# Performance work log

Measured on AMD Instinct MI355X. Metric: run time of the kernel, lower is better.

Reference implementation:

```python
import jax, jax.numpy as jnp
import numpy as np

N_NODES = 50000
N_EDGES = 800000
N_REL = 16
D = 64          # entity_dim == relation_dim == n_hidden
NEG_SLOPE = 0.01  # torch F.leaky_relu default


def setup_inputs() -> dict:
    key = jax.random.key(0)
    ks = jax.random.split(key, 12)
    s = 1.0 / np.sqrt(D)
    return {
        "node_ids": jnp.arange(N_NODES, dtype=jnp.int64) if jax.config.jax_enable_x64 else jnp.arange(N_NODES, dtype=jnp.int32),
        "relation_ids": jax.random.randint(ks[0], (N_EDGES,), 0, N_REL),
        "src": jax.random.randint(ks[1], (N_EDGES,), 0, N_NODES),
        "dst": jax.random.randint(ks[2], (N_EDGES,), 0, N_NODES),
        "entity_embed": jax.random.normal(ks[3], (N_NODES, D), jnp.float32) * s,
        "relation_embed": jax.random.normal(ks[4], (N_REL, D), jnp.float32) * s,
        "W0": jax.random.normal(ks[5], (N_REL, D, D), jnp.float32) * s,
        "W1": jax.random.normal(ks[6], (N_REL, D, D), jnp.float32) * s,
        "ra0": jax.random.normal(ks[7], (D, D), jnp.float32) * s,
        "rb0": jax.random.normal(ks[8], (D, D), jnp.float32) * s,
        "ra1": jax.random.normal(ks[9], (D, D), jnp.float32) * s,
        "rb1": jax.random.normal(ks[10], (D, D), jnp.float32) * s,
    }


def _edge_softmax(scores, dst, n_nodes):
    # segment softmax over edges grouped by destination node (DGL edge_softmax)
    m = jax.ops.segment_max(scores, dst, num_segments=n_nodes)  # [N]
    e = jnp.exp(scores - m[dst])                                # [E]
    z = jax.ops.segment_sum(e, dst, num_segments=n_nodes)       # [N]
    return e / z[dst]


def _kgat_layer(h, efeat, src, dst, etype, Wr, ra, rb, n_nodes):
    # transform every node under every relation once: [N, R, Dr]
    trans = jnp.einsum('nd,rde->nre', h, Wr)
    t_r = trans[src, etype]                   # W_r h_t  [E, Dr]
    h_r = trans[dst, etype]                   # W_r h_h  [E, Dr]
    att = jnp.sum(t_r * jnp.tanh(h_r + efeat), axis=1)  # [E]
    a = _edge_softmax(att, dst, n_nodes)                 # [E]
    # u_mul_e + sum: scatter-add weighted source features to dst
    h_nb = jax.ops.segment_sum(h[src] * a[:, None], dst, num_segments=n_nodes)
    # Bi residual
    out = (jax.nn.leaky_relu((h + h_nb) @ ra, NEG_SLOPE)
           + jax.nn.leaky_relu((h * h_nb) @ rb, NEG_SLOPE))
    return out


def reference(node_ids, relation_ids, src, dst, entity_embed, relation_embed,
              W0, W1, ra0, rb0, ra1, rb1):
    h = entity_embed[node_ids]                 # [N, D]
    efeat = relation_embed[relation_ids]       # [E, D]
    n_nodes = node_ids.shape[0]
    cache = [h]
    for Wr, ra, rb in ((W0, ra0, rb0), (W1, ra1, rb1)):
        h = _kgat_layer(h, efeat, src, dst, relation_ids, Wr, ra, rb, n_nodes)
        cache.append(h)
    return jnp.concatenate(cache, axis=1)      # [N, 3*D]
```

## Files before the change

### kernel.cpp

```cpp
#include <hip/hip_runtime.h>
#include <hip/hip_bf16.h>
#include <math.h>

#define NN 50000
#define NE 800000
#define NR 16
#define DD 64
#define OSTRIDE 192
#define QSTRIDE 1032

typedef __attribute__((ext_vector_type(8))) short bf16x8;
typedef __attribute__((ext_vector_type(4))) float f32x4;

__device__ inline float tanh_fast(float x) {
    return 1.f - 2.f / (__expf(2.f * x) + 1.f);
}
__device__ inline unsigned short f2bf(float f) {
    unsigned u = __float_as_uint(f);
    return (unsigned short)((u + 0x7fffu + ((u >> 16) & 1u)) >> 16);
}
__device__ inline float bf2f(unsigned short s) {
    return __uint_as_float((unsigned)s << 16);
}

__global__ void k_deg(const int* __restrict__ dst, int* __restrict__ cnt) {
    for (int e = blockIdx.x * blockDim.x + threadIdx.x; e < NE;
         e += gridDim.x * blockDim.x)
        atomicAdd(&cnt[dst[e]], 1);
}

__global__ __launch_bounds__(256) void k_scan1(const int* __restrict__ cnt,
                                               int* __restrict__ rowptr,
                                               int* __restrict__ bsum) {
    __shared__ int sh[256];
    int b = blockIdx.x, t = threadIdx.x;
    int i = b * 256 + t;
    int v = (i < NN) ? cnt[i] : 0;
    sh[t] = v;
    __syncthreads();
    #pragma unroll
    for (int o = 1; o < 256; o <<= 1) {
        int u = (t >= o) ? sh[t - o] : 0;
        __syncthreads();
        sh[t] += u;
        __syncthreads();
    }
    if (i < NN) rowptr[i] = sh[t] - v;
    if (t == 255) bsum[b] = sh[255];
}

__global__ __launch_bounds__(256) void k_scan2(int* __restrict__ bsum, int nb) {
    __shared__ int sh[256];
    int t = threadIdx.x;
    int v = (t < nb) ? bsum[t] : 0;
    sh[t] = v;
    __syncthreads();
    #pragma unroll
    for (int o = 1; o < 256; o <<= 1) {
        int u = (t >= o) ? sh[t - o] : 0;
        __syncthreads();
        sh[t] += u;
        __syncthreads();
    }
    if (t < nb) bsum[t] = sh[t] - v;
}

__global__ __launch_bounds__(256) void k_scan3(int* __restrict__ rowptr,
                                               const int* __restrict__ bsum,
                                               int* __restrict__ cursor) {
    int b = blockIdx.x, t = threadIdx.x;
    int i = b * 256 + t;
    if (i < NN) {
        int v = rowptr[i] + bsum[b];
        rowptr[i] = v;
        cursor[i] = v;
    }
    if (i == 0) rowptr[NN] = NE;
}

__global__ void k_fill(const int* __restrict__ dst, const int* __restrict__ src,
                       const int* __restrict__ rel, int* __restrict__ cursor,
                       int* __restrict__ epack) {
    for (int e = blockIdx.x * blockDim.x + threadIdx.x; e < NE;
         e += gridDim.x * blockDim.x) {
        int pos = atomicAdd(&cursor[dst[e]], 1);
        epack[pos] = src[e] | (rel[e] << 16);
    }
}

__global__ void k_copy_h0(const int* __restrict__ node_ids,
                          const float* __restrict__ ent,
                          float* __restrict__ out,
                          unsigned short* __restrict__ hbf) {
    int i = blockIdx.x * blockDim.x + threadIdx.x;
    if (i >= NN * DD) return;
    int n = i >> 6, d = i & 63;
    float v = ent[(size_t)node_ids[n] * DD + d];
    out[(size_t)n * OSTRIDE + d] = v;
    hbf[(size_t)n * DD + d] = f2bf(v);
}

__global__ void k_wprep(const float* __restrict__ W, unsigned short* __restrict__ wbf,
                        unsigned short* __restrict__ wtbf) {
    int i = blockIdx.x * blockDim.x + threadIdx.x;
    if (i >= NR * DD * DD) return;
    int r = i >> 12, rem = i & 4095, d = rem >> 6, E = rem & 63;
    unsigned short v = f2bf(W[i]);
    wbf[i] = v;
    wtbf[(r << 12) | (E << 6) | d] = v;
}

__global__ __launch_bounds__(1024) void k_fused7(const unsigned short* __restrict__ hbf,
                                                 const unsigned short* __restrict__ wbf,
                                                 const unsigned short* __restrict__ wtbf,
                                                 const float* __restrict__ relE,
                                                 const int* __restrict__ rowptr,
                                                 const int* __restrict__ epack,
                                                 float* __restrict__ h_nb) {
    __shared__ __align__(16) unsigned short q_lds[16 * QSTRIDE];
    __shared__ __align__(16) unsigned short u_lds[16][16][72];
    int n0 = blockIdx.x * 16;
    int t  = threadIdx.x;
    int w  = t >> 6, l = t & 63;
    int l15 = l & 15, lg = l >> 4;
    int r = w;

    {
        int ar = n0 + l15; if (ar >= NN) ar = NN - 1;
        const unsigned short* ap = hbf + (size_t)ar * DD + lg * 8;
        bf16x8 a0 = *(const bf16x8*)ap;
        bf16x8 a1 = *(const bf16x8*)(ap + 32);

        f32x4 acc[4];
        #pragma unroll
        for (int nt = 0; nt < 4; ++nt) acc[nt] = (f32x4){0.f, 0.f, 0.f, 0.f};
        const unsigned short* wtr = wtbf + (r << 12);
        #pragma unroll
        for (int nt = 0; nt < 4; ++nt) {
            const unsigned short* bp = wtr + (nt * 16 + l15) * DD + lg * 8;
            bf16x8 b0 = *(const bf16x8*)bp;
            bf16x8 b1 = *(const bf16x8*)(bp + 32);
            acc[nt] = __builtin_amdgcn_mfma_f32_16x16x32_bf16(a0, b0, acc[nt], 0, 0, 0);
            acc[nt] = __builtin_amdgcn_mfma_f32_16x16x32_bf16(a1, b1, acc[nt], 0, 0, 0);
        }

        #pragma unroll
        for (int nt = 0; nt < 4; ++nt) {
            int E = nt * 16 + l15;
            float er = relE[r * DD + E];
            #pragma unroll
            for (int reg = 0; reg < 4; ++reg)
                u_lds[w][lg * 4 + reg][E] = f2bf(tanh_fast(acc[nt][reg] + er));
        }
        asm volatile("s_waitcnt lgkmcnt(0)" ::: "memory");

        const unsigned short* up = &u_lds[w][l15][lg * 8];
        bf16x8 u0 = *(const bf16x8*)up;
        bf16x8 u1 = *(const bf16x8*)(up + 32);

        f32x4 q4[4];
        #pragma unroll
        for (int nt = 0; nt < 4; ++nt) q4[nt] = (f32x4){0.f, 0.f, 0.f, 0.f};
        const unsigned short* wr = wbf + (r << 12);
        #pragma unroll
        for (int nt = 0; nt < 4; ++nt) {
            const unsigned short* bp = wr + (nt * 16 + l15) * DD + lg * 8;
            bf16x8 b0 = *(const bf16x8*)bp;
            bf16x8 b1 = *(const bf16x8*)(bp + 32);
            q4[nt] = __builtin_amdgcn_mfma_f32_16x16x32_bf16(u0, b0, q4[nt], 0, 0, 0);
            q4[nt] = __builtin_amdgcn_mfma_f32_16x16x32_bf16(u1, b1, q4[nt], 0, 0, 0);
        }

        #pragma unroll
        for (int reg = 0; reg < 4; ++reg) {
            unsigned short* qp = q_lds + (lg * 4 + reg) * QSTRIDE + r * 64 + l15;
            #pragma unroll
            for (int nt = 0; nt < 4; ++nt)
                qp[nt * 16] = f2bf(q4[nt][reg]);
        }
    }
    __syncthreads();

    int n = n0 + w;
    if (n >= NN) return;
    const unsigned short* ql = q_lds + w * QSTRIDE;
    int row0 = rowptr[n], row1 = rowptr[n + 1];
    int deg = row1 - row0;
    int g = lg;

    const float NEGBIG = -1e30f;
    float m = NEGBIG, zr = 0.f;
    float a0 = 0.f, a1 = 0.f, a2 = 0.f, a3 = 0.f;

    int steps = (deg + 3) >> 2;
    for (int k = 0; k < steps; ++k) {
        int idx = row0 + (k << 2) + g;
        bool ok = idx < row1;
        int p = epack[ok ? idx : row0];
        int s = p & 0xffff, rr = p >> 16;
        uint2 hu = *(const uint2*)(hbf + ((size_t)s << 6) + (l15 << 2));
        uint2 qu = *(const uint2*)(ql + rr * 64 + (l15 << 2));
        float h0 = __uint_as_float(hu.x << 16);
        float h1 = __uint_as_float(hu.x & 0xffff0000u);
        float h2 = __uint_as_float(hu.y << 16);
        float h3 = __uint_as_float(hu.y & 0xffff0000u);
        float q0 = __uint_as_float(qu.x << 16);
        float q1 = __uint_as_float(qu.x & 0xffff0000u);
        float q2 = __uint_as_float(qu.y << 16);
        float q3 = __uint_as_float(qu.y & 0xffff0000u);
        float d = h0 * q0 + h1 * q1 + h2 * q2 + h3 * q3;
        d += __shfl_xor(d, 1, 64);
        d += __shfl_xor(d, 2, 64);
        d += __shfl_xor(d, 4, 64);
        d += __shfl_xor(d, 8, 64);
        float v  = ok ? d : NEGBIG;
        float mn = fmaxf(m, v);
        float sc = __expf(m - mn);
        float wg = ok ? __expf(v - mn) : 0.f;
        zr = zr * sc + wg;
        a0 = a0 * sc + wg * h0;
        a1 = a1 * sc + wg * h1;
        a2 = a2 * sc + wg * h2;
        a3 = a3 * sc + wg * h3;
        m = mn;
    }

    float mo = fmaxf(m, __shfl_xor(m, 16, 64));
    float ms = fmaxf(mo, __shfl_xor(mo, 32, 64));
    float scg = __expf(m - ms);
    zr *= scg; a0 *= scg; a1 *= scg; a2 *= scg; a3 *= scg;
    zr += __shfl_xor(zr, 16, 64); zr += __shfl_xor(zr, 32, 64);
    a0 += __shfl_xor(a0, 16, 64); a0 += __shfl_xor(a0, 32, 64);
    a1 += __shfl_xor(a1, 16, 64); a1 += __shfl_xor(a1, 32, 64);
    a2 += __shfl_xor(a2, 16, 64); a2 += __shfl_xor(a2, 32, 64);
    a3 += __shfl_xor(a3, 16, 64); a3 += __shfl_xor(a3, 32, 64);

    if (g == 0) {
        float inv = (deg > 0) ? 1.f / zr : 0.f;
        float4 o = make_float4(a0 * inv, a1 * inv, a2 * inv, a3 * inv);
        *(float4*)&h_nb[((size_t)n << 6) + (l15 << 2)] = o;
    }
}

__global__ __launch_bounds__(256) void k_out2(const float* __restrict__ h_nb,
                                              const float* __restrict__ ra,
                                              const float* __restrict__ rb,
                                              float* __restrict__ out,
                                              int off_in, int off_out,
                                              unsigned short* __restrict__ hbf) {
    __shared__ __align__(16) float v1s[64][68];
    __shared__ __align__(16) float v2s[64][68];
    __shared__ __align__(16) float ws[2][64][64];
    int t = threadIdx.x;
    int n0 = blockIdx.x * 64;

    for (int i = t; i < 1024; i += 256) {
        int ni = i >> 4, c4 = (i & 15) * 4;
        int n = n0 + ni;
        float4 hv = make_float4(0.f, 0.f, 0.f, 0.f);
        float4 nb = make_float4(0.f, 0.f, 0.f, 0.f);
        if (n < NN) {
            hv = *(const float4*)&out[(size_t)n * OSTRIDE + off_in + c4];
            nb = *(const float4*)&h_nb[(size_t)n * DD + c4];
        }
        v1s[c4 + 0][ni] = hv.x + nb.x;  v2s[c4 + 0][ni] = hv.x * nb.x;
        v1s[c4 + 1][ni] = hv.y + nb.y;  v2s[c4 + 1][ni] = hv.y * nb.y;
        v1s[c4 + 2][ni] = hv.z + nb.z;  v2s[c4 + 2][ni] = hv.z * nb.z;
        v1s[c4 + 3][ni] = hv.w + nb.w;  v2s[c4 + 3][ni] = hv.w * nb.w;
    }
    for (int i = t; i < 2048; i += 256) {
        const float* base = (i < 1024) ? ra : rb;
        int rem = i & 1023;
        float4 v = *(const float4*)&base[rem * 4];
        int k = rem >> 4, c4 = (rem & 15) * 4;
        *(float4*)&ws[i >> 10][k][c4] = v;
    }
    __syncthreads();

    int nd0 = (t >> 4) * 4;
    int c0  = (t & 15) * 4;
    float a1[4][4] = {}, a2[4][4] = {};
    #pragma unroll 8
    for (int k = 0; k < 64; ++k) {
        float4 h1 = *(const float4*)&v1s[k][nd0];
        float4 h2 = *(const float4*)&v2s[k][nd0];
        float4 wa = *(const float4*)&ws[0][k][c0];
        float4 wb = *(const float4*)&ws[1][k][c0];
        float x1[4] = {h1.x, h1.y, h1.z, h1.w};
        float x2[4] = {h2.x, h2.y, h2.z, h2.w};
        #pragma unroll
        for (int i = 0; i < 4; ++i) {
            a1[i][0] += x1[i] * wa.x; a1[i][1] += x1[i] * wa.y;
            a1[i][2] += x1[i] * wa.z; a1[i][3] += x1[i] * wa.w;
            a2[i][0] += x2[i] * wb.x; a2[i][1] += x2[i] * wb.y;
            a2[i][2] += x2[i] * wb.z; a2[i][3] += x2[i] * wb.w;
        }
    }
    #pragma unroll
    for (int i = 0; i < 4; ++i) {
        int n = n0 + nd0 + i;
        if (n >= NN) continue;
        float4 o;
        float* po = (float*)&o;
        #pragma unroll
        for (int j = 0; j < 4; ++j) {
            float u1 = a1[i][j], u2 = a2[i][j];
            u1 = u1 > 0.f ? u1 : 0.01f * u1;
            u2 = u2 > 0.f ? u2 : 0.01f * u2;
            po[j] = u1 + u2;
        }
        *(float4*)&out[(size_t)n * OSTRIDE + off_out + c0] = o;
        hbf[(size_t)n * DD + c0 + 0] = f2bf(o.x);
        hbf[(size_t)n * DD + c0 + 1] = f2bf(o.y);
        hbf[(size_t)n * DD + c0 + 2] = f2bf(o.z);
        hbf[(size_t)n * DD + c0 + 3] = f2bf(o.w);
    }
}

extern "C" void kernel_launch(void* const* d_in, const int* in_sizes, int n_in,
                              void* d_out, int out_size, void* d_ws, size_t ws_size,
                              hipStream_t stream) {
    const int*   node_ids = (const int*)d_in[0];
    const int*   rel_ids  = (const int*)d_in[1];
    const int*   src      = (const int*)d_in[2];
    const int*   dst      = (const int*)d_in[3];
    const float* ent      = (const float*)d_in[4];
    const float* relE     = (const float*)d_in[5];
    const float* W[2]  = {(const float*)d_in[6], (const float*)d_in[7]};
    const float* ra[2] = {(const float*)d_in[8], (const float*)d_in[10]};
    const float* rb[2] = {(const float*)d_in[9], (const float*)d_in[11]};
    float* out = (float*)d_out;

    const size_t hnb_bytes    = (size_t)NN * DD * sizeof(float);
    const size_t hbf_bytes    = (size_t)NN * DD * sizeof(short);
    const size_t wbf_bytes    = (size_t)NR * DD * DD * sizeof(short);
    const size_t epack_bytes  = (size_t)NE * sizeof(int);
    const size_t rowptr_bytes = (size_t)(NN + 1) * sizeof(int);
    const size_t cnt_bytes    = (size_t)NN * sizeof(int);
    const int    NB_SCAN      = (NN + 255) / 256;
    const size_t bsum_bytes   = (size_t)256 * sizeof(int);

    char* p = (char*)d_ws;
    float*          h_nb   = (float*)p;          p += hnb_bytes;
    unsigned short* hbf    = (unsigned short*)p; p += hbf_bytes;
    unsigned short* wbf    = (unsigned short*)p; p += wbf_bytes;
    unsigned short* wtbf   = (unsigned short*)p; p += wbf_bytes;
    int*            epack  = (int*)p;            p += epack_bytes;
    int*            rowptr = (int*)p;            p += rowptr_bytes;
    int*            cnt    = (int*)p;            p += cnt_bytes;
    int*            bsum   = (int*)p;            p += bsum_bytes;
    (void)ws_size;

    hipMemsetAsync(cnt, 0, cnt_bytes, stream);
    k_deg  <<<1024, 256, 0, stream>>>(dst, cnt);
    k_scan1<<<NB_SCAN, 256, 0, stream>>>(cnt, rowptr, bsum);
    k_scan2<<<1, 256, 0, stream>>>(bsum, NB_SCAN);
    k_scan3<<<NB_SCAN, 256, 0, stream>>>(rowptr, bsum, cnt);
    k_fill <<<1024, 256, 0, stream>>>(dst, src, rel_ids, cnt, epack);

    k_copy_h0<<<(NN * DD + 255) / 256, 256, 0, stream>>>(node_ids, ent, out, hbf);

    for (int L = 0; L < 2; ++L) {
        int off_in = L * DD;
        int off_out = (L + 1) * DD;

        k_wprep <<<(NR * DD * DD + 255) / 256, 256, 0, stream>>>(W[L], wbf, wtbf);
        k_fused7<<<(NN + 15) / 16, 1024, 0, stream>>>(hbf, wbf, wtbf, relE,
                                                      rowptr, epack, h_nb);
        k_out2  <<<(NN + 63) / 64, 256, 0, stream>>>(h_nb, ra[L], rb[L], out,
                                                     off_in, off_out, hbf);
    }
}
```

Baseline: 434.8 us.

## Switch to fp16 storage with dot2 and drop online softmax max-tracking

Converts node features, weights and the per-edge q vectors from bf16 to fp16 and uses fp16 MFMA plus fdot2 for the attention dot products. The edge loop now has each lane handle 8 features and processes 8 edges per step instead of 4, giving wider 16-byte gathers and a shorter shuffle reduction. The running-max rescaling of the online softmax is removed and raw exp of the scores is summed directly. This cuts per-edge ALU and exp work, but risks fp16 range overflow in the features or in exp if scores grow large.

```diff
diff --git a/kernel.cpp b/kernel.cpp
--- a/kernel.cpp
+++ b/kernel.cpp
@@ -9,18 +9,21 @@
 #define OSTRIDE 192
 #define QSTRIDE 1032
 
-typedef __attribute__((ext_vector_type(8))) short bf16x8;
+typedef _Float16 f16;
+typedef f16 f16x8 __attribute__((ext_vector_type(8)));
+typedef f16 f16x2 __attribute__((ext_vector_type(2)));
 typedef __attribute__((ext_vector_type(4))) float f32x4;
 
 __device__ inline float tanh_fast(float x) {
     return 1.f - 2.f / (__expf(2.f * x) + 1.f);
 }
-__device__ inline unsigned short f2bf(float f) {
-    unsigned u = __float_as_uint(f);
-    return (unsigned short)((u + 0x7fffu + ((u >> 16) & 1u)) >> 16);
-}
-__device__ inline float bf2f(unsigned short s) {
-    return __uint_as_float((unsigned)s << 16);
+
+__device__ inline float dot2acc(f16x2 a, f16x2 b, float c) {
+#if __has_builtin(__builtin_amdgcn_fdot2)
+    return __builtin_amdgcn_fdot2(a, b, c, false);
+#else
+    return c + (float)a[0] * (float)b[0] + (float)a[1] * (float)b[1];
+#endif
 }
 
 __global__ void k_deg(const int* __restrict__ dst, int* __restrict__ cnt) {
@@ -91,34 +94,34 @@
 __global__ void k_copy_h0(const int* __restrict__ node_ids,
                           const float* __restrict__ ent,
                           float* __restrict__ out,
-                          unsigned short* __restrict__ hbf) {
+                          f16* __restrict__ hf) {
     int i = blockIdx.x * blockDim.x + threadIdx.x;
     if (i >= NN * DD) return;
     int n = i >> 6, d = i & 63;
     float v = ent[(size_t)node_ids[n] * DD + d];
     out[(size_t)n * OSTRIDE + d] = v;
-    hbf[(size_t)n * DD + d] = f2bf(v);
-}
-
-__global__ void k_wprep(const float* __restrict__ W, unsigned short* __restrict__ wbf,
-                        unsigned short* __restrict__ wtbf) {
+    hf[(size_t)n * DD + d] = (f16)v;
+}
+
+__global__ void k_wprep(const float* __restrict__ W, f16* __restrict__ wf,
+                        f16* __restrict__ wtf) {
     int i = blockIdx.x * blockDim.x + threadIdx.x;
     if (i >= NR * DD * DD) return;
     int r = i >> 12, rem = i & 4095, d = rem >> 6, E = rem & 63;
-    unsigned short v = f2bf(W[i]);
-    wbf[i] = v;
-    wtbf[(r << 12) | (E << 6) | d] = v;
-}
-
-__global__ __launch_bounds__(1024) void k_fused7(const unsigned short* __restrict__ hbf,
-                                                 const unsigned short* __restrict__ wbf,
-                                                 const unsigned short* __restrict__ wtbf,
+    f16 v = (f16)W[i];
+    wf[i] = v;
+    wtf[(r << 12) | (E << 6) | d] = v;
+}
+
+__global__ __launch_bounds__(1024) void k_fused8(const f16* __restrict__ hf,
+                                                 const f16* __restrict__ wf,
+                                                 const f16* __restrict__ wtf,
                                                  const float* __restrict__ relE,
                                                  const int* __restrict__ rowptr,
                                                  const int* __restrict__ epack,
                                                  float* __restrict__ h_nb) {
-    __shared__ __align__(16) unsigned short q_lds[16 * QSTRIDE];
-    __shared__ __align__(16) unsigned short u_lds[16][16][72];
+    __shared__ __align__(16) f16 q_lds[16 * QSTRIDE];
+    __shared__ __align__(16) f16 u_lds[16][16][72];
     int n0 = blockIdx.x * 16;
     int t  = threadIdx.x;
     int w  = t >> 6, l = t & 63;
@@ -127,21 +130,21 @@
 
     {
         int ar = n0 + l15; if (ar >= NN) ar = NN - 1;
-        const unsigned short* ap = hbf + (size_t)ar * DD + lg * 8;
-        bf16x8 a0 = *(const bf16x8*)ap;
-        bf16x8 a1 = *(const bf16x8*)(ap + 32);
+        const f16* ap = hf + (size_t)ar * DD + lg * 8;
+        f16x8 a0 = *(const f16x8*)ap;
+        f16x8 a1 = *(const f16x8*)(ap + 32);
 
         f32x4 acc[4];
         #pragma unroll
         for (int nt = 0; nt < 4; ++nt) acc[nt] = (f32x4){0.f, 0.f, 0.f, 0.f};
-        const unsigned short* wtr = wtbf + (r << 12);
+        const f16* wtr = wtf + (r << 12);
         #pragma unroll
         for (int nt = 0; nt < 4; ++nt) {
-            const unsigned short* bp = wtr + (nt * 16 + l15) * DD + lg * 8;
-            bf16x8 b0 = *(const bf16x8*)bp;
-            bf16x8 b1 = *(const bf16x8*)(bp + 32);
-            acc[nt] = __builtin_amdgcn_mfma_f32_16x16x32_bf16(a0, b0, acc[nt], 0, 0, 0);
-            acc[nt] = __builtin_amdgcn_mfma_f32_16x16x32_bf16(a1, b1, acc[nt], 0, 0, 0);
+            const f16* bp = wtr + (nt * 16 + l15) * DD + lg * 8;
+            f16x8 b0 = *(const f16x8*)bp;
+            f16x8 b1 = *(const f16x8*)(bp + 32);
+            acc[nt] = __builtin_amdgcn_mfma_f32_16x16x32_f16(a0, b0, acc[nt], 0, 0, 0);
+            acc[nt] = __builtin_amdgcn_mfma_f32_16x16x32_f16(a1, b1, acc[nt], 0, 0, 0);
         }
 
         #pragma unroll
@@ -150,95 +153,86 @@
             float er = relE[r * DD + E];
             #pragma unroll
             for (int reg = 0; reg < 4; ++reg)
-                u_lds[w][lg * 4 + reg][E] = f2bf(tanh_fast(acc[nt][reg] + er));
+                u_lds[w][lg * 4 + reg][E] = (f16)tanh_fast(acc[nt][reg] + er);
         }
         asm volatile("s_waitcnt lgkmcnt(0)" ::: "memory");
 
-        const unsigned short* up = &u_lds[w][l15][lg * 8];
-        bf16x8 u0 = *(const bf16x8*)up;
-        bf16x8 u1 = *(const bf16x8*)(up + 32);
+        const f16* up = &u_lds[w][l15][lg * 8];
+        f16x8 u0 = *(const f16x8*)up;
+        f16x8 u1 = *(const f16x8*)(up + 32);
 
         f32x4 q4[4];
         #pragma unroll
         for (int nt = 0; nt < 4; ++nt) q4[nt] = (f32x4){0.f, 0.f, 0.f, 0.f};
-        const unsigned short* wr = wbf + (r << 12);
+        const f16* wr = wf + (r << 12);
         #pragma unroll
         for (int nt = 0; nt < 4; ++nt) {
-            const unsigned short* bp = wr + (nt * 16 + l15) * DD + lg * 8;
-            bf16x8 b0 = *(const bf16x8*)bp;
-            bf16x8 b1 = *(const bf16x8*)(bp + 32);
-            q4[nt] = __builtin_amdgcn_mfma_f32_16x16x32_bf16(u0, b0, q4[nt], 0, 0, 0);
-            q4[nt] = __builtin_amdgcn_mfma_f32_16x16x32_bf16(u1, b1, q4[nt], 0, 0, 0);
+            const f16* bp = wr + (nt * 16 + l15) * DD + lg * 8;
+            f16x8 b0 = *(const f16x8*)bp;
+            f16x8 b1 = *(const f16x8*)(bp + 32);
+            q4[nt] = __builtin_amdgcn_mfma_f32_16x16x32_f16(u0, b0, q4[nt], 0, 0, 0);
+            q4[nt] = __builtin_amdgcn_mfma_f32_16x16x32_f16(u1, b1, q4[nt], 0, 0, 0);
         }
 
         #pragma unroll
         for (int reg = 0; reg < 4; ++reg) {
-            unsigned short* qp = q_lds + (lg * 4 + reg) * QSTRIDE + r * 64 + l15;
+            f16* qp = q_lds + (lg * 4 + reg) * QSTRIDE + r * 64 + l15;
             #pragma unroll
             for (int nt = 0; nt < 4; ++nt)
-                qp[nt * 16] = f2bf(q4[nt][reg]);
+                qp[nt * 16] = (f16)q4[nt][reg];
         }
     }
     __syncthreads();
 
     int n = n0 + w;
     if (n >= NN) return;
-    const unsigned short* ql = q_lds + w * QSTRIDE;
+    const f16* ql = q_lds + w * QSTRIDE;
     int row0 = rowptr[n], row1 = rowptr[n + 1];
     int deg = row1 - row0;
-    int g = lg;
-
-    const float NEGBIG = -1e30f;
-    float m = NEGBIG, zr = 0.f;
-    float a0 = 0.f, a1 = 0.f, a2 = 0.f, a3 = 0.f;
-
-    int steps = (deg + 3) >> 2;
+    int g  = l >> 3;
+    int d8 = l & 7;
+
+    float zr = 0.f;
+    float a[8] = {};
+
+    int steps = (deg + 7) >> 3;
     for (int k = 0; k < steps; ++k) {
-        int idx = row0 + (k << 2) + g;
+        int idx = row0 + (k << 3) + g;
         bool ok = idx < row1;
         int p = epack[ok ? idx : row0];
         int s = p & 0xffff, rr = p >> 16;
-        uint2 hu = *(const uint2*)(hbf + ((size_t)s << 6) + (l15 << 2));
-        uint2 qu = *(const uint2*)(ql + rr * 64 + (l15 << 2));
-        float h0 = __uint_as_float(hu.x << 16);
-        float h1 = __uint_as_float(hu.x & 0xffff0000u);
-        float h2 = __uint_as_float(hu.y << 16);
-        float h3 = __uint_as_float(hu.y & 0xffff0000u);
-        float q0 = __uint_as_float(qu.x << 16);
-        float q1 = __uint_as_float(qu.x & 0xffff0000u);
-        float q2 = __uint_as_float(qu.y << 16);
-        float q3 = __uint_as_float(qu.y & 0xffff0000u);
-        float d = h0 * q0 + h1 * q1 + h2 * q2 + h3 * q3;
-        d += __shfl_xor(d, 1, 64);
-        d += __shfl_xor(d, 2, 64);
-        d += __shfl_xor(d, 4, 64);
-        d += __shfl_xor(d, 8, 64);
-        float v  = ok ? d : NEGBIG;
-        float mn = fmaxf(m, v);
-        float sc = __expf(m - mn);
-        float wg = ok ? __expf(v - mn) : 0.f;
-        zr = zr * sc + wg;
-        a0 = a0 * sc + wg * h0;
-        a1 = a1 * sc + wg * h1;
-        a2 = a2 * sc + wg * h2;
-        a3 = a3 * sc + wg * h3;
-        m = mn;
-    }
-
-    float mo = fmaxf(m, __shfl_xor(m, 16, 64));
-    float ms = fmaxf(mo, __shfl_xor(mo, 32, 64));
-    float scg = __expf(m - ms);
-    zr *= scg; a0 *= scg; a1 *= scg; a2 *= scg; a3 *= scg;
-    zr += __shfl_xor(zr, 16, 64); zr += __shfl_xor(zr, 32, 64);
-    a0 += __shfl_xor(a0, 16, 64); a0 += __shfl_xor(a0, 32, 64);
-    a1 += __shfl_xor(a1, 16, 64); a1 += __shfl_xor(a1, 32, 64);
-    a2 += __shfl_xor(a2, 16, 64); a2 += __shfl_xor(a2, 32, 64);
-    a3 += __shfl_xor(a3, 16, 64); a3 += __shfl_xor(a3, 32, 64);
+        f16x8 hv = *(const f16x8*)(hf + ((size_t)s << 6) + (d8 << 3));
+        f16x8 qv = *(const f16x8*)(ql + (rr << 6) + (d8 << 3));
+        float dp = 0.f;
+        #pragma unroll
+        for (int j = 0; j < 4; ++j) {
+            f16x2 ha = {hv[2 * j], hv[2 * j + 1]};
+            f16x2 qa = {qv[2 * j], qv[2 * j + 1]};
+            dp = dot2acc(ha, qa, dp);
+        }
+        dp += __shfl_xor(dp, 1, 64);
+        dp += __shfl_xor(dp, 2, 64);
+        dp += __shfl_xor(dp, 4, 64);
+        float wg = ok ? __expf(dp) : 0.f;
+        zr += wg;
+        #pragma unroll
+        for (int j = 0; j < 8; ++j)
+            a[j] = fmaf(wg, (float)hv[j], a[j]);
+    }
+
+    #pragma unroll
+    for (int o = 8; o < 64; o <<= 1) {
+        zr += __shfl_xor(zr, o, 64);
+        #pragma unroll
+        for (int j = 0; j < 8; ++j)
+            a[j] += __shfl_xor(a[j], o, 64);
+    }
 
     if (g == 0) {
         float inv = (deg > 0) ? 1.f / zr : 0.f;
-        float4 o = make_float4(a0 * inv, a1 * inv, a2 * inv, a3 * inv);
-        *(float4*)&h_nb[((size_t)n << 6) + (l15 << 2)] = o;
+        float4* dst4 = (float4*)&h_nb[((size_t)n << 6) + (d8 << 3)];
+        dst4[0] = make_float4(a[0] * inv, a[1] * inv, a[2] * inv, a[3] * inv);
+        dst4[1] = make_float4(a[4] * inv, a[5] * inv, a[6] * inv, a[7] * inv);
     }
 }
 
@@ -247,7 +241,7 @@
                                               const float* __restrict__ rb,
                                               float* __restrict__ out,
                                               int off_in, int off_out,
-                                              unsigned short* __restrict__ hbf) {
+                                              f16* __restrict__ hf) {
     __shared__ __align__(16) float v1s[64][68];
     __shared__ __align__(16) float v2s[64][68];
     __shared__ __align__(16) float ws[2][64][64];
@@ -310,10 +304,10 @@
             po[j] = u1 + u2;
         }
         *(float4*)&out[(size_t)n * OSTRIDE + off_out + c0] = o;
-        hbf[(size_t)n * DD + c0 + 0] = f2bf(o.x);
-        hbf[(size_t)n * DD + c0 + 1] = f2bf(o.y);
-        hbf[(size_t)n * DD + c0 + 2] = f2bf(o.z);
-        hbf[(size_t)n * DD + c0 + 3] = f2bf(o.w);
+        hf[(size_t)n * DD + c0 + 0] = (f16)o.x;
+        hf[(size_t)n * DD + c0 + 1] = (f16)o.y;
+        hf[(size_t)n * DD + c0 + 2] = (f16)o.z;
+        hf[(size_t)n * DD + c0 + 3] = (f16)o.w;
     }
 }
 
@@ -332,8 +326,8 @@
     float* out = (float*)d_out;
 
     const size_t hnb_bytes    = (size_t)NN * DD * sizeof(float);
-    const size_t hbf_bytes    = (size_t)NN * DD * sizeof(short);
-    const size_t wbf_bytes    = (size_t)NR * DD * DD * sizeof(short);
+    const size_t hf_bytes     = (size_t)NN * DD * sizeof(f16);
+    const size_t wf_bytes     = (size_t)NR * DD * DD * sizeof(f16);
     const size_t epack_bytes  = (size_t)NE * sizeof(int);
     const size_t rowptr_bytes = (size_t)(NN + 1) * sizeof(int);
     const size_t cnt_bytes    = (size_t)NN * sizeof(int);
@@ -341,14 +335,14 @@
     const size_t bsum_bytes   = (size_t)256 * sizeof(int);
 
     char* p = (char*)d_ws;
-    float*          h_nb   = (float*)p;          p += hnb_bytes;
-    unsigned short* hbf    = (unsigned short*)p; p += hbf_bytes;
-    unsigned short* wbf    = (unsigned short*)p; p += wbf_bytes;
-    unsigned short* wtbf   = (unsigned short*)p; p += wbf_bytes;
-    int*            epack  = (int*)p;            p += epack_bytes;
-    int*            rowptr = (int*)p;            p += rowptr_bytes;
-    int*            cnt    = (int*)p;            p += cnt_bytes;
-    int*            bsum   = (int*)p;            p += bsum_bytes;
+    float* h_nb   = (float*)p; p += hnb_bytes;
+    f16*   hf     = (f16*)p;   p += hf_bytes;
+    f16*   wf     = (f16*)p;   p += wf_bytes;
+    f16*   wtf    = (f16*)p;   p += wf_bytes;
+    int*   epack  = (int*)p;   p += epack_bytes;
+    int*   rowptr = (int*)p;   p += rowptr_bytes;
+    int*   cnt    = (int*)p;   p += cnt_bytes;
+    int*   bsum   = (int*)p;   p += bsum_bytes;
     (void)ws_size;
 
     hipMemsetAsync(cnt, 0, cnt_bytes, stream);
@@ -358,16 +352,16 @@
     k_scan3<<<NB_SCAN, 256, 0, stream>>>(rowptr, bsum, cnt);
     k_fill <<<1024, 256, 0, stream>>>(dst, src, rel_ids, cnt, epack);
 
-    k_copy_h0<<<(NN * DD + 255) / 256, 256, 0, stream>>>(node_ids, ent, out, hbf);
+    k_copy_h0<<<(NN * DD + 255) / 256, 256, 0, stream>>>(node_ids, ent, out, hf);
 
     for (int L = 0; L < 2; ++L) {
         int off_in = L * DD;
         int off_out = (L + 1) * DD;
 
-        k_wprep <<<(NR * DD * DD + 255) / 256, 256, 0, stream>>>(W[L], wbf, wtbf);
-        k_fused7<<<(NN + 15) / 16, 1024, 0, stream>>>(hbf, wbf, wtbf, relE,
+        k_wprep <<<(NR * DD * DD + 255) / 256, 256, 0, stream>>>(W[L], wf, wtf);
+        k_fused8<<<(NN + 15) / 16, 1024, 0, stream>>>(hf, wf, wtf, relE,
                                                       rowptr, epack, h_nb);
         k_out2  <<<(NN + 63) / 64, 256, 0, stream>>>(h_nb, ra[L], rb[L], out,
-                                                     off_in, off_out, hbf);
-    }
-}
+                                                     off_in, off_out, hf);
+    }
+}
```

New measurement: 412.2 us. 1.05x faster.
